# Kernel optimization log

Hardware: AMD Instinct MI355X
Metric: run time of the kernel (lower is better)

The kernel has to match this reference:

```python
import jax, jax.numpy as jnp
import numpy as np

ALPHA = 0.2  # leaky-relu negative slope AND the residual scale self.alpha

def setup_inputs() -> dict:
    key = jax.random.key(0)
    k1, k2, k3 = jax.random.split(key, 3)
    B, N, C_in, C_out = 8, 2048, 128, 128
    text = jax.random.normal(k1, (B, N, C_in), dtype=jnp.float32)
    adj = jnp.ones((B, N, N), dtype=jnp.float32)  # unused by the layer's forward
    W = jax.random.normal(k2, (C_in, C_out), dtype=jnp.float32) * (1.414 / np.sqrt(C_in + C_out))
    a = jax.random.normal(k3, (2 * C_out, 1), dtype=jnp.float32) * (1.414 / np.sqrt(2 * C_out + 1))
    return {"text": text, "adj": adj, "W": W, "a": a}

def reference(text, adj, W, a):
    # text: [B,N,C_in]; adj is unused (faithful to the source forward).
    h = jnp.einsum('bnc,cf->bnf', text, W)                  # [B,N,F]
    F_out = W.shape[1]
    a1 = a[:F_out, 0]                                       # score contribution of node i
    a2 = a[F_out:, 0]                                       # score contribution of node j
    s1 = jnp.einsum('bnf,f->bn', h, a1)                     # [B,N]
    s2 = jnp.einsum('bnf,f->bn', h, a2)                     # [B,N]
    # leakyrelu(cat(h_i,h_j) @ a) == leakyrelu(s1_i + s2_j): avoids O(N^2*2F) concat
    e = jax.nn.leaky_relu(s1[:, :, None] + s2[:, None, :], negative_slope=ALPHA)  # [B,N,N]
    attention = jax.nn.softmax(e, axis=2)                   # dropout is a no-op in eval mode
    h_prime = jnp.einsum('bij,bjf->bif', attention, h)      # [B,N,F]
    return jax.nn.elu(h_prime + ALPHA * h)
```

## Files before the change

kernel.cpp:

```cpp
#include <hip/hip_runtime.h>
#include <hip/hip_bf16.h>
#include <math.h>

#define LRELU_ALPHA 0.2f

constexpr int B_ = 8;
constexpr int N_ = 2048;
constexpr int M_ = B_ * N_;
constexpr int SEG = 32;
constexpr int NSEG = N_ / SEG;

__global__ __launch_bounds__(512) void k_gemm(const float* __restrict__ text,
                                              const float* __restrict__ W,
                                              const float* __restrict__ a,
                                              float* __restrict__ h,
                                              float* __restrict__ s1,
                                              float* __restrict__ s2,
                                              float* __restrict__ eN0,
                                              float* __restrict__ eP0) {
    __shared__ float As[64 * 33];
    __shared__ float Ws[32 * 128];
    const int tid = threadIdx.x;
    const int r0  = blockIdx.x * 64;
    const int cx  = tid & 15;
    const int ry  = tid >> 4;
    const int c0  = cx * 8;
    const int rr0 = ry * 2;

    float acc[2][8];
#pragma unroll
    for (int i = 0; i < 2; ++i)
#pragma unroll
        for (int j = 0; j < 8; ++j) acc[i][j] = 0.f;

    for (int kk = 0; kk < 128; kk += 32) {
        for (int idx = tid; idx < 64 * 32; idx += 512) {
            int r = idx >> 5, c = idx & 31;
            As[r * 33 + c] = text[(r0 + r) * 128 + kk + c];
        }
        for (int idx = tid; idx < 32 * 128; idx += 512) {
            int k = idx >> 7, f = idx & 127;
            Ws[k * 128 + f] = W[(kk + k) * 128 + f];
        }
        __syncthreads();
#pragma unroll
        for (int k = 0; k < 32; ++k) {
            float4 w0 = *(const float4*)&Ws[k * 128 + c0];
            float4 w1 = *(const float4*)&Ws[k * 128 + c0 + 4];
#pragma unroll
            for (int i = 0; i < 2; ++i) {
                float av = As[(rr0 + i) * 33 + k];
                acc[i][0] += av * w0.x; acc[i][1] += av * w0.y;
                acc[i][2] += av * w0.z; acc[i][3] += av * w0.w;
                acc[i][4] += av * w1.x; acc[i][5] += av * w1.y;
                acc[i][6] += av * w1.z; acc[i][7] += av * w1.w;
            }
        }
        __syncthreads();
    }

    float4 a10 = *(const float4*)&a[c0];
    float4 a11 = *(const float4*)&a[c0 + 4];
    float4 a20 = *(const float4*)&a[128 + c0];
    float4 a21 = *(const float4*)&a[128 + c0 + 4];

#pragma unroll
    for (int i = 0; i < 2; ++i) {
        int row = r0 + rr0 + i;
        float4 o0 = {acc[i][0], acc[i][1], acc[i][2], acc[i][3]};
        float4 o1 = {acc[i][4], acc[i][5], acc[i][6], acc[i][7]};
        *(float4*)&h[row * 128 + c0]     = o0;
        *(float4*)&h[row * 128 + c0 + 4] = o1;

        float p1 = o0.x * a10.x + o0.y * a10.y + o0.z * a10.z + o0.w * a10.w
                 + o1.x * a11.x + o1.y * a11.y + o1.z * a11.z + o1.w * a11.w;
        float p2 = o0.x * a20.x + o0.y * a20.y + o0.z * a20.z + o0.w * a20.w
                 + o1.x * a21.x + o1.y * a21.y + o1.z * a21.z + o1.w * a21.w;
#pragma unroll
        for (int off = 8; off >= 1; off >>= 1) {
            p1 += __shfl_xor(p1, off);
            p2 += __shfl_xor(p2, off);
        }
        if (cx == 0) {
            s1[row] = p1;
            s2[row] = p2;
            eN0[row] = expf(LRELU_ALPHA * p2);
            eP0[row] = expf(p2);
        }
    }
}

__global__ __launch_bounds__(512) void k_rank(const float* __restrict__ s2,
                                              const float* __restrict__ eN0,
                                              const float* __restrict__ eP0,
                                              const float* __restrict__ s1,
                                              int* __restrict__ perm,
                                              float* __restrict__ eNs,
                                              float* __restrict__ ePs,
                                              int* __restrict__ rank,
                                              float* __restrict__ ZN,
                                              float* __restrict__ ZP) {
    __shared__ float ls2[2048], leN[2048], leP[2048];
    __shared__ int   redc[512], redm[512];
    __shared__ float redn[512], redp[512];

    const int b  = blockIdx.x >> 5;
    const int eb = blockIdx.x & 31;
    const int tid = threadIdx.x;
    const int e = tid & 63;
    const int c = tid >> 6;

    {
        const float4* g2 = (const float4*)(s2  + b * 2048);
        const float4* gn = (const float4*)(eN0 + b * 2048);
        const float4* gp = (const float4*)(eP0 + b * 2048);
        ((float4*)ls2)[tid] = g2[tid];
        ((float4*)leN)[tid] = gn[tid];
        ((float4*)leP)[tid] = gp[tid];
    }
    __syncthreads();

    const int i  = eb * 64 + e;
    const int gi = b * 2048 + i;
    const float myS2 = ls2[i];
    const float thr  = -s1[gi];

    int cnt = 0, mr = 0;
    float sn = 0.f, sp = 0.f;
    const int j0 = c * 256;
#pragma unroll 4
    for (int j = j0; j < j0 + 256; j += 4) {
        float4 v  = *(const float4*)&ls2[j];
        float4 en = *(const float4*)&leN[j];
        float4 ep = *(const float4*)&leP[j];
#define PROC(vv, ee, pp, jj)                                             \
        { bool le = (vv) <= thr;                                         \
          cnt += le ? 1 : 0;                                             \
          sn  += le ? (ee) : 0.f;                                        \
          sp  += le ? 0.f : (pp);                                        \
          mr  += ((vv) < myS2 || ((vv) == myS2 && (jj) < i)) ? 1 : 0; }
        PROC(v.x, en.x, ep.x, j + 0)
        PROC(v.y, en.y, ep.y, j + 1)
        PROC(v.z, en.z, ep.z, j + 2)
        PROC(v.w, en.w, ep.w, j + 3)
#undef PROC
    }
    redc[tid] = cnt; redm[tid] = mr; redn[tid] = sn; redp[tid] = sp;
    __syncthreads();
    if (c == 0) {
        int tc = 0, tm = 0; float tn = 0.f, tp = 0.f;
#pragma unroll
        for (int cc = 0; cc < 8; ++cc) {
            tc += redc[cc * 64 + e];
            tm += redm[cc * 64 + e];
            tn += redn[cc * 64 + e];
            tp += redp[cc * 64 + e];
        }
        perm[b * 2048 + tm] = i;
        eNs [b * 2048 + tm] = leN[i];
        ePs [b * 2048 + tm] = leP[i];
        rank[gi] = tc;
        ZN[gi] = tn;
        ZP[gi] = tp;
    }
}

__global__ __launch_bounds__(128) void k_segsum(const float* __restrict__ h,
                                                const int* __restrict__ perm,
                                                const float* __restrict__ eNs,
                                                const float* __restrict__ ePs,
                                                float* __restrict__ segN,
                                                float* __restrict__ segP) {
    const int blk = blockIdx.x;
    const int b = blk >> 6, s = blk & 63;
    const int f = threadIdx.x;
    const int rbase = s * SEG;
    float an = 0.f, ap = 0.f;
#pragma unroll 4
    for (int r = 0; r < SEG; ++r) {
        int rr = b * 2048 + rbase + r;
        float hv = h[(b * 2048 + perm[rr]) * 128 + f];
        an += eNs[rr] * hv;
        ap += ePs[rr] * hv;
    }
    segN[blk * 128 + f] = an;
    segP[blk * 128 + f] = ap;
}

__global__ __launch_bounds__(128) void k_prefix(const float* __restrict__ h,
                                                const int* __restrict__ perm,
                                                const float* __restrict__ eNs,
                                                const float* __restrict__ ePs,
                                                const float* __restrict__ segN,
                                                const float* __restrict__ segP,
                                                __hip_bfloat16* __restrict__ Pre,
                                                __hip_bfloat16* __restrict__ Suf) {
    const int blk = blockIdx.x;
    const int b = blk >> 6, s = blk & 63;
    const int f = threadIdx.x;
    const int rbase = s * SEG;

    float an = 0.f, ap = 0.f;
    for (int ss = 0; ss < s; ++ss)        an += segN[(b * NSEG + ss) * 128 + f];
    for (int ss = s + 1; ss < NSEG; ++ss) ap += segP[(b * NSEG + ss) * 128 + f];

    float hv[SEG];
#pragma unroll
    for (int r = 0; r < SEG; ++r) {
        int rr = b * 2048 + rbase + r;
        hv[r] = h[(b * 2048 + perm[rr]) * 128 + f];
        Pre[(size_t)(b * 2049 + rbase + r) * 128 + f] = __float2bfloat16(an);
        an += eNs[rr] * hv[r];
    }
#pragma unroll
    for (int r = SEG - 1; r >= 0; --r) {
        int rr = b * 2048 + rbase + r;
        ap += ePs[rr] * hv[r];
        Suf[(size_t)(b * 2049 + rbase + r) * 128 + f] = __float2bfloat16(ap);
    }
    if (s == NSEG - 1) {
        Pre[(size_t)(b * 2049 + 2048) * 128 + f] = __float2bfloat16(an);
        Suf[(size_t)(b * 2049 + 2048) * 128 + f] = __float2bfloat16(0.f);
    }
}

__global__ __launch_bounds__(256) void k_out(const float* __restrict__ h,
                                             const float* __restrict__ s1,
                                             const int* __restrict__ rank,
                                             const float* __restrict__ ZN,
                                             const float* __restrict__ ZP,
                                             const __hip_bfloat16* __restrict__ Pre,
                                             const __hip_bfloat16* __restrict__ Suf,
                                             float* __restrict__ out) {
    const int tid = threadIdx.x;
    const int lr = tid >> 7, f = tid & 127;
    const int i = blockIdx.x * 2 + lr;
    const int b = i >> 11;

    const float s1v = s1[i];
    const float E1 = expf(s1v);
    const float E2 = expf(LRELU_ALPHA * s1v);
    const int   r  = rank[i];
    const float Z  = E1 * ZP[i] + E2 * ZN[i];
    const size_t o = (size_t)(b * 2049 + r) * 128 + f;
    const float hp = (E1 * __bfloat162float(Suf[o]) + E2 * __bfloat162float(Pre[o])) / Z;
    const float x = hp + LRELU_ALPHA * h[i * 128 + f];
    out[i * 128 + f] = (x > 0.f) ? x : expm1f(x);
}

extern "C" void kernel_launch(void* const* d_in, const int* in_sizes, int n_in,
                              void* d_out, int out_size, void* d_ws, size_t ws_size,
                              hipStream_t stream) {
    const float* text = (const float*)d_in[0];
    const float* W = (const float*)d_in[2];
    const float* a = (const float*)d_in[3];
    float* out = (float*)d_out;

    float* p = (float*)d_ws;
    float* h    = p; p += (size_t)M_ * 128;
    float* s1   = p; p += M_;
    float* s2   = p; p += M_;
    float* eN0  = p; p += M_;
    float* eP0  = p; p += M_;
    int*   perm = (int*)p; p += M_;
    float* eNs  = p; p += M_;
    float* ePs  = p; p += M_;
    int*   rank = (int*)p; p += M_;
    float* ZN   = p; p += M_;
    float* ZP   = p; p += M_;
    float* segN = p; p += B_ * NSEG * 128;
    float* segP = p; p += B_ * NSEG * 128;
    __hip_bfloat16* Pre = (__hip_bfloat16*)p; p += (size_t)B_ * 2049 * 128 / 2;
    __hip_bfloat16* Suf = (__hip_bfloat16*)p; p += (size_t)B_ * 2049 * 128 / 2;

    hipLaunchKernelGGL(k_gemm,   dim3(M_ / 64),   dim3(512), 0, stream,
                       text, W, a, h, s1, s2, eN0, eP0);
    hipLaunchKernelGGL(k_rank,   dim3(B_ * 32),   dim3(512), 0, stream,
                       s2, eN0, eP0, s1, perm, eNs, ePs, rank, ZN, ZP);
    hipLaunchKernelGGL(k_segsum, dim3(B_ * NSEG), dim3(128), 0, stream,
                       h, perm, eNs, ePs, segN, segP);
    hipLaunchKernelGGL(k_prefix, dim3(B_ * NSEG), dim3(128), 0, stream,
                       h, perm, eNs, ePs, segN, segP, Pre, Suf);
    hipLaunchKernelGGL(k_out,    dim3(M_ / 2),    dim3(256), 0, stream,
                       h, s1, rank, ZN, ZP, Pre, Suf, out);
}
```

Measured before the change: 235.4 us.

## Fuse all five stages into one cooperative persistent kernel with grid syncs

Replaces the five separate launches (gemm, rank, segment sums, prefix/suffix scans, output) with a single cooperative kernel of 256 blocks that separates stages with grid-wide syncs and reuses one shared-memory union across phases. The GEMM phase is retiled to 64-wide k chunks with a transposed A tile and 4x8 register tiles, computed by only half the threads. The segment-sum and scan phases are rebalanced so each block handles two segments, with the prefix and suffix scans split across thread halves. The aim is to remove launch gaps and tail effects between kernels, at the cost of grid-sync overhead, idle threads in the GEMM, and only 256 blocks doing the output stage.

```diff
diff --git a/kernel.cpp b/kernel.cpp
--- a/kernel.cpp
+++ b/kernel.cpp
@@ -1,6 +1,9 @@
 #include <hip/hip_runtime.h>
 #include <hip/hip_bf16.h>
+#include <hip/hip_cooperative_groups.h>
 #include <math.h>
+
+namespace cg = cooperative_groups;
 
 #define LRELU_ALPHA 0.2f
 
@@ -10,242 +13,241 @@
 constexpr int SEG = 32;
 constexpr int NSEG = N_ / SEG;
 
-__global__ __launch_bounds__(512) void k_gemm(const float* __restrict__ text,
-                                              const float* __restrict__ W,
-                                              const float* __restrict__ a,
-                                              float* __restrict__ h,
-                                              float* __restrict__ s1,
-                                              float* __restrict__ s2,
-                                              float* __restrict__ eN0,
-                                              float* __restrict__ eP0) {
-    __shared__ float As[64 * 33];
-    __shared__ float Ws[32 * 128];
+__global__ __launch_bounds__(512) void k_fused(
+    const float* __restrict__ text, const float* __restrict__ W,
+    const float* __restrict__ a,
+    float* __restrict__ h, float* __restrict__ s1, float* __restrict__ s2,
+    float* __restrict__ eN0, float* __restrict__ eP0,
+    int* __restrict__ perm, float* __restrict__ eNs, float* __restrict__ ePs,
+    int* __restrict__ rank, float* __restrict__ ZN, float* __restrict__ ZP,
+    float* __restrict__ segN, float* __restrict__ segP,
+    __hip_bfloat16* __restrict__ Pre, __hip_bfloat16* __restrict__ Suf,
+    float* __restrict__ out) {
+
+    __shared__ __align__(16) union {
+        struct { float Ast[64 * 68]; float Ws[64 * 128]; } p1;
+        struct { float ls2[2048], leN[2048], leP[2048];
+                 int redc[512], redm[512]; float redn[512], redp[512]; } p2;
+        struct { float an[512], ap[512]; } p3;
+    } sm;
+
     const int tid = threadIdx.x;
-    const int r0  = blockIdx.x * 64;
-    const int cx  = tid & 15;
-    const int ry  = tid >> 4;
-    const int c0  = cx * 8;
-    const int rr0 = ry * 2;
-
-    float acc[2][8];
-#pragma unroll
-    for (int i = 0; i < 2; ++i)
-#pragma unroll
-        for (int j = 0; j < 8; ++j) acc[i][j] = 0.f;
-
-    for (int kk = 0; kk < 128; kk += 32) {
-        for (int idx = tid; idx < 64 * 32; idx += 512) {
-            int r = idx >> 5, c = idx & 31;
-            As[r * 33 + c] = text[(r0 + r) * 128 + kk + c];
-        }
-        for (int idx = tid; idx < 32 * 128; idx += 512) {
-            int k = idx >> 7, f = idx & 127;
-            Ws[k * 128 + f] = W[(kk + k) * 128 + f];
+    const int blk = blockIdx.x;
+    cg::grid_group grid = cg::this_grid();
+
+    {
+        const int r0 = blk * 64;
+        const int cx = tid & 15;
+        const int ry = tid >> 4;
+        const int c0 = cx * 4;
+        const int c1 = 64 + cx * 4;
+        const int rr0 = ry * 4;
+
+        float acc[4][8];
+#pragma unroll
+        for (int i = 0; i < 4; ++i)
+#pragma unroll
+            for (int j = 0; j < 8; ++j) acc[i][j] = 0.f;
+
+        for (int kk = 0; kk < 128; kk += 64) {
+            for (int idx = tid; idx < 64 * 64; idx += 512) {
+                int r = idx >> 6, k = idx & 63;
+                sm.p1.Ast[k * 68 + r] = text[(size_t)(r0 + r) * 128 + kk + k];
+            }
+            for (int idx = tid; idx < 64 * 128; idx += 512) {
+                int k = idx >> 7, f = idx & 127;
+                sm.p1.Ws[k * 128 + f] = W[(kk + k) * 128 + f];
+            }
+            __syncthreads();
+            if (tid < 256) {
+#pragma unroll 16
+                for (int k = 0; k < 64; ++k) {
+                    float4 av = *(const float4*)&sm.p1.Ast[k * 68 + rr0];
+                    float4 w0 = *(const float4*)&sm.p1.Ws[k * 128 + c0];
+                    float4 w1 = *(const float4*)&sm.p1.Ws[k * 128 + c1];
+                    const float avv[4] = {av.x, av.y, av.z, av.w};
+#pragma unroll
+                    for (int i = 0; i < 4; ++i) {
+                        acc[i][0] += avv[i] * w0.x; acc[i][1] += avv[i] * w0.y;
+                        acc[i][2] += avv[i] * w0.z; acc[i][3] += avv[i] * w0.w;
+                        acc[i][4] += avv[i] * w1.x; acc[i][5] += avv[i] * w1.y;
+                        acc[i][6] += avv[i] * w1.z; acc[i][7] += avv[i] * w1.w;
+                    }
+                }
+            }
+            __syncthreads();
+        }
+
+        if (tid < 256) {
+            float4 a1lo = *(const float4*)&a[c0];
+            float4 a1hi = *(const float4*)&a[c1];
+            float4 a2lo = *(const float4*)&a[128 + c0];
+            float4 a2hi = *(const float4*)&a[128 + c1];
+#pragma unroll
+            for (int i = 0; i < 4; ++i) {
+                const int row = r0 + rr0 + i;
+                float4 o0 = {acc[i][0], acc[i][1], acc[i][2], acc[i][3]};
+                float4 o1 = {acc[i][4], acc[i][5], acc[i][6], acc[i][7]};
+                *(float4*)&h[(size_t)row * 128 + c0] = o0;
+                *(float4*)&h[(size_t)row * 128 + c1] = o1;
+
+                float p1 = o0.x*a1lo.x + o0.y*a1lo.y + o0.z*a1lo.z + o0.w*a1lo.w
+                         + o1.x*a1hi.x + o1.y*a1hi.y + o1.z*a1hi.z + o1.w*a1hi.w;
+                float p2 = o0.x*a2lo.x + o0.y*a2lo.y + o0.z*a2lo.z + o0.w*a2lo.w
+                         + o1.x*a2hi.x + o1.y*a2hi.y + o1.z*a2hi.z + o1.w*a2hi.w;
+#pragma unroll
+                for (int off = 8; off >= 1; off >>= 1) {
+                    p1 += __shfl_xor(p1, off);
+                    p2 += __shfl_xor(p2, off);
+                }
+                if (cx == 0) {
+                    s1[row] = p1;
+                    s2[row] = p2;
+                    eN0[row] = expf(LRELU_ALPHA * p2);
+                    eP0[row] = expf(p2);
+                }
+            }
+        }
+    }
+    grid.sync();
+
+    {
+        const int b  = blk >> 5;
+        const int eb = blk & 31;
+        const int e  = tid & 63;
+        const int c  = tid >> 6;
+        {
+            const float4* g2 = (const float4*)(s2  + b * 2048);
+            const float4* gn = (const float4*)(eN0 + b * 2048);
+            const float4* gp = (const float4*)(eP0 + b * 2048);
+            ((float4*)sm.p2.ls2)[tid] = g2[tid];
+            ((float4*)sm.p2.leN)[tid] = gn[tid];
+            ((float4*)sm.p2.leP)[tid] = gp[tid];
         }
         __syncthreads();
-#pragma unroll
-        for (int k = 0; k < 32; ++k) {
-            float4 w0 = *(const float4*)&Ws[k * 128 + c0];
-            float4 w1 = *(const float4*)&Ws[k * 128 + c0 + 4];
-#pragma unroll
-            for (int i = 0; i < 2; ++i) {
-                float av = As[(rr0 + i) * 33 + k];
-                acc[i][0] += av * w0.x; acc[i][1] += av * w0.y;
-                acc[i][2] += av * w0.z; acc[i][3] += av * w0.w;
-                acc[i][4] += av * w1.x; acc[i][5] += av * w1.y;
-                acc[i][6] += av * w1.z; acc[i][7] += av * w1.w;
-            }
-        }
+
+        const int i  = eb * 64 + e;
+        const int gi = b * 2048 + i;
+        const float myS2 = sm.p2.ls2[i];
+        const float thr  = -s1[gi];
+
+        int cnt = 0, mr = 0;
+        float sn = 0.f, sp = 0.f;
+        const int j0 = c * 256;
+#pragma unroll 4
+        for (int j = j0; j < j0 + 256; j += 4) {
+            float4 v  = *(const float4*)&sm.p2.ls2[j];
+            float4 en = *(const float4*)&sm.p2.leN[j];
+            float4 ep = *(const float4*)&sm.p2.leP[j];
+#define PROC(vv, ee, pp, jj)                                             \
+            { bool le = (vv) <= thr;                                     \
+              cnt += le ? 1 : 0;                                         \
+              sn  += le ? (ee) : 0.f;                                    \
+              sp  += le ? 0.f : (pp);                                    \
+              mr  += ((vv) < myS2 || ((vv) == myS2 && (jj) < i)) ? 1 : 0; }
+            PROC(v.x, en.x, ep.x, j + 0)
+            PROC(v.y, en.y, ep.y, j + 1)
+            PROC(v.z, en.z, ep.z, j + 2)
+            PROC(v.w, en.w, ep.w, j + 3)
+#undef PROC
+        }
+        sm.p2.redc[tid] = cnt; sm.p2.redm[tid] = mr;
+        sm.p2.redn[tid] = sn;  sm.p2.redp[tid] = sp;
         __syncthreads();
-    }
-
-    float4 a10 = *(const float4*)&a[c0];
-    float4 a11 = *(const float4*)&a[c0 + 4];
-    float4 a20 = *(const float4*)&a[128 + c0];
-    float4 a21 = *(const float4*)&a[128 + c0 + 4];
-
-#pragma unroll
-    for (int i = 0; i < 2; ++i) {
-        int row = r0 + rr0 + i;
-        float4 o0 = {acc[i][0], acc[i][1], acc[i][2], acc[i][3]};
-        float4 o1 = {acc[i][4], acc[i][5], acc[i][6], acc[i][7]};
-        *(float4*)&h[row * 128 + c0]     = o0;
-        *(float4*)&h[row * 128 + c0 + 4] = o1;
-
-        float p1 = o0.x * a10.x + o0.y * a10.y + o0.z * a10.z + o0.w * a10.w
-                 + o1.x * a11.x + o1.y * a11.y + o1.z * a11.z + o1.w * a11.w;
-        float p2 = o0.x * a20.x + o0.y * a20.y + o0.z * a20.z + o0.w * a20.w
-                 + o1.x * a21.x + o1.y * a21.y + o1.z * a21.z + o1.w * a21.w;
-#pragma unroll
-        for (int off = 8; off >= 1; off >>= 1) {
-            p1 += __shfl_xor(p1, off);
-            p2 += __shfl_xor(p2, off);
-        }
-        if (cx == 0) {
-            s1[row] = p1;
-            s2[row] = p2;
-            eN0[row] = expf(LRELU_ALPHA * p2);
-            eP0[row] = expf(p2);
-        }
-    }
-}
-
-__global__ __launch_bounds__(512) void k_rank(const float* __restrict__ s2,
-                                              const float* __restrict__ eN0,
-                                              const float* __restrict__ eP0,
-                                              const float* __restrict__ s1,
-                                              int* __restrict__ perm,
-                                              float* __restrict__ eNs,
-                                              float* __restrict__ ePs,
-                                              int* __restrict__ rank,
-                                              float* __restrict__ ZN,
-                                              float* __restrict__ ZP) {
-    __shared__ float ls2[2048], leN[2048], leP[2048];
-    __shared__ int   redc[512], redm[512];
-    __shared__ float redn[512], redp[512];
-
-    const int b  = blockIdx.x >> 5;
-    const int eb = blockIdx.x & 31;
-    const int tid = threadIdx.x;
-    const int e = tid & 63;
-    const int c = tid >> 6;
-
-    {
-        const float4* g2 = (const float4*)(s2  + b * 2048);
-        const float4* gn = (const float4*)(eN0 + b * 2048);
-        const float4* gp = (const float4*)(eP0 + b * 2048);
-        ((float4*)ls2)[tid] = g2[tid];
-        ((float4*)leN)[tid] = gn[tid];
-        ((float4*)leP)[tid] = gp[tid];
-    }
-    __syncthreads();
-
-    const int i  = eb * 64 + e;
-    const int gi = b * 2048 + i;
-    const float myS2 = ls2[i];
-    const float thr  = -s1[gi];
-
-    int cnt = 0, mr = 0;
-    float sn = 0.f, sp = 0.f;
-    const int j0 = c * 256;
-#pragma unroll 4
-    for (int j = j0; j < j0 + 256; j += 4) {
-        float4 v  = *(const float4*)&ls2[j];
-        float4 en = *(const float4*)&leN[j];
-        float4 ep = *(const float4*)&leP[j];
-#define PROC(vv, ee, pp, jj)                                             \
-        { bool le = (vv) <= thr;                                         \
-          cnt += le ? 1 : 0;                                             \
-          sn  += le ? (ee) : 0.f;                                        \
-          sp  += le ? 0.f : (pp);                                        \
-          mr  += ((vv) < myS2 || ((vv) == myS2 && (jj) < i)) ? 1 : 0; }
-        PROC(v.x, en.x, ep.x, j + 0)
-        PROC(v.y, en.y, ep.y, j + 1)
-        PROC(v.z, en.z, ep.z, j + 2)
-        PROC(v.w, en.w, ep.w, j + 3)
-#undef PROC
-    }
-    redc[tid] = cnt; redm[tid] = mr; redn[tid] = sn; redp[tid] = sp;
-    __syncthreads();
-    if (c == 0) {
-        int tc = 0, tm = 0; float tn = 0.f, tp = 0.f;
-#pragma unroll
-        for (int cc = 0; cc < 8; ++cc) {
-            tc += redc[cc * 64 + e];
-            tm += redm[cc * 64 + e];
-            tn += redn[cc * 64 + e];
-            tp += redp[cc * 64 + e];
-        }
-        perm[b * 2048 + tm] = i;
-        eNs [b * 2048 + tm] = leN[i];
-        ePs [b * 2048 + tm] = leP[i];
-        rank[gi] = tc;
-        ZN[gi] = tn;
-        ZP[gi] = tp;
-    }
-}
-
-__global__ __launch_bounds__(128) void k_segsum(const float* __restrict__ h,
-                                                const int* __restrict__ perm,
-                                                const float* __restrict__ eNs,
-                                                const float* __restrict__ ePs,
-                                                float* __restrict__ segN,
-                                                float* __restrict__ segP) {
-    const int blk = blockIdx.x;
-    const int b = blk >> 6, s = blk & 63;
-    const int f = threadIdx.x;
-    const int rbase = s * SEG;
-    float an = 0.f, ap = 0.f;
-#pragma unroll 4
-    for (int r = 0; r < SEG; ++r) {
-        int rr = b * 2048 + rbase + r;
-        float hv = h[(b * 2048 + perm[rr]) * 128 + f];
-        an += eNs[rr] * hv;
-        ap += ePs[rr] * hv;
-    }
-    segN[blk * 128 + f] = an;
-    segP[blk * 128 + f] = ap;
-}
-
-__global__ __launch_bounds__(128) void k_prefix(const float* __restrict__ h,
-                                                const int* __restrict__ perm,
-                                                const float* __restrict__ eNs,
-                                                const float* __restrict__ ePs,
-                                                const float* __restrict__ segN,
-                                                const float* __restrict__ segP,
-                                                __hip_bfloat16* __restrict__ Pre,
-                                                __hip_bfloat16* __restrict__ Suf) {
-    const int blk = blockIdx.x;
-    const int b = blk >> 6, s = blk & 63;
-    const int f = threadIdx.x;
-    const int rbase = s * SEG;
-
-    float an = 0.f, ap = 0.f;
-    for (int ss = 0; ss < s; ++ss)        an += segN[(b * NSEG + ss) * 128 + f];
-    for (int ss = s + 1; ss < NSEG; ++ss) ap += segP[(b * NSEG + ss) * 128 + f];
-
-    float hv[SEG];
-#pragma unroll
-    for (int r = 0; r < SEG; ++r) {
-        int rr = b * 2048 + rbase + r;
-        hv[r] = h[(b * 2048 + perm[rr]) * 128 + f];
-        Pre[(size_t)(b * 2049 + rbase + r) * 128 + f] = __float2bfloat16(an);
-        an += eNs[rr] * hv[r];
-    }
-#pragma unroll
-    for (int r = SEG - 1; r >= 0; --r) {
-        int rr = b * 2048 + rbase + r;
-        ap += ePs[rr] * hv[r];
-        Suf[(size_t)(b * 2049 + rbase + r) * 128 + f] = __float2bfloat16(ap);
-    }
-    if (s == NSEG - 1) {
-        Pre[(size_t)(b * 2049 + 2048) * 128 + f] = __float2bfloat16(an);
-        Suf[(size_t)(b * 2049 + 2048) * 128 + f] = __float2bfloat16(0.f);
-    }
-}
-
-__global__ __launch_bounds__(256) void k_out(const float* __restrict__ h,
-                                             const float* __restrict__ s1,
-                                             const int* __restrict__ rank,
-                                             const float* __restrict__ ZN,
-                                             const float* __restrict__ ZP,
-                                             const __hip_bfloat16* __restrict__ Pre,
-                                             const __hip_bfloat16* __restrict__ Suf,
-                                             float* __restrict__ out) {
-    const int tid = threadIdx.x;
-    const int lr = tid >> 7, f = tid & 127;
-    const int i = blockIdx.x * 2 + lr;
-    const int b = i >> 11;
-
-    const float s1v = s1[i];
-    const float E1 = expf(s1v);
-    const float E2 = expf(LRELU_ALPHA * s1v);
-    const int   r  = rank[i];
-    const float Z  = E1 * ZP[i] + E2 * ZN[i];
-    const size_t o = (size_t)(b * 2049 + r) * 128 + f;
-    const float hp = (E1 * __bfloat162float(Suf[o]) + E2 * __bfloat162float(Pre[o])) / Z;
-    const float x = hp + LRELU_ALPHA * h[i * 128 + f];
-    out[i * 128 + f] = (x > 0.f) ? x : expm1f(x);
+        if (c == 0) {
+            int tc = 0, tm = 0; float tn = 0.f, tp = 0.f;
+#pragma unroll
+            for (int cc = 0; cc < 8; ++cc) {
+                tc += sm.p2.redc[cc * 64 + e];
+                tm += sm.p2.redm[cc * 64 + e];
+                tn += sm.p2.redn[cc * 64 + e];
+                tp += sm.p2.redp[cc * 64 + e];
+            }
+            perm[b * 2048 + tm] = i;
+            eNs [b * 2048 + tm] = sm.p2.leN[i];
+            ePs [b * 2048 + tm] = sm.p2.leP[i];
+            rank[gi] = tc;
+            ZN[gi] = tn;
+            ZP[gi] = tp;
+        }
+    }
+    grid.sync();
+
+    {
+        const int task = blk * 2 + (tid >> 8);
+        const int st = tid & 255;
+        const int f  = st & 127;
+        const int hf = st >> 7;
+        const int b3 = task >> 6, s3 = task & 63;
+        float an = 0.f, ap = 0.f;
+        const int rb = b3 * 2048 + s3 * SEG + hf * 16;
+#pragma unroll 4
+        for (int r = 0; r < 16; ++r) {
+            int rr = rb + r;
+            float hv = h[(size_t)(b3 * 2048 + perm[rr]) * 128 + f];
+            an += eNs[rr] * hv;
+            ap += ePs[rr] * hv;
+        }
+        sm.p3.an[tid] = an; sm.p3.ap[tid] = ap;
+        __syncthreads();
+        if (hf == 0) {
+            segN[task * 128 + f] = sm.p3.an[tid] + sm.p3.an[tid + 128];
+            segP[task * 128 + f] = sm.p3.ap[tid] + sm.p3.ap[tid + 128];
+        }
+    }
+    grid.sync();
+
+    {
+        const int task = blk * 2 + (tid >> 8);
+        const int st = tid & 255;
+        const int f  = st & 127;
+        const int hf = st >> 7;
+        const int b4 = task >> 6, s4 = task & 63;
+        const int rbase = s4 * SEG;
+        if (hf == 0) {
+            float an = 0.f;
+            for (int ss = 0; ss < s4; ++ss) an += segN[(b4 * NSEG + ss) * 128 + f];
+#pragma unroll 4
+            for (int r = 0; r < SEG; ++r) {
+                int rr = b4 * 2048 + rbase + r;
+                Pre[(size_t)(b4 * 2049 + rbase + r) * 128 + f] = __float2bfloat16(an);
+                an += eNs[rr] * h[(size_t)(b4 * 2048 + perm[rr]) * 128 + f];
+            }
+            if (s4 == NSEG - 1)
+                Pre[(size_t)(b4 * 2049 + 2048) * 128 + f] = __float2bfloat16(an);
+        } else {
+            float ap = 0.f;
+            for (int ss = s4 + 1; ss < NSEG; ++ss) ap += segP[(b4 * NSEG + ss) * 128 + f];
+#pragma unroll 4
+            for (int r = SEG - 1; r >= 0; --r) {
+                int rr = b4 * 2048 + rbase + r;
+                ap += ePs[rr] * h[(size_t)(b4 * 2048 + perm[rr]) * 128 + f];
+                Suf[(size_t)(b4 * 2049 + rbase + r) * 128 + f] = __float2bfloat16(ap);
+            }
+            if (s4 == NSEG - 1)
+                Suf[(size_t)(b4 * 2049 + 2048) * 128 + f] = __float2bfloat16(0.f);
+        }
+    }
+    grid.sync();
+
+    {
+        const int lr = tid >> 7;
+        const int f  = tid & 127;
+#pragma unroll 2
+        for (int it = 0; it < 16; ++it) {
+            const int i = blk * 64 + it * 4 + lr;
+            const int b = i >> 11;
+            const float s1v = s1[i];
+            const float E1 = expf(s1v);
+            const float E2 = expf(LRELU_ALPHA * s1v);
+            const int   r  = rank[i];
+            const float Z  = E1 * ZP[i] + E2 * ZN[i];
+            const size_t o = (size_t)(b * 2049 + r) * 128 + f;
+            const float hp = (E1 * __bfloat162float(Suf[o]) + E2 * __bfloat162float(Pre[o])) / Z;
+            const float x = hp + LRELU_ALPHA * h[(size_t)i * 128 + f];
+            out[(size_t)i * 128 + f] = (x > 0.f) ? x : expm1f(x);
+        }
+    }
 }
 
 extern "C" void kernel_launch(void* const* d_in, const int* in_sizes, int n_in,
@@ -273,14 +275,9 @@
     __hip_bfloat16* Pre = (__hip_bfloat16*)p; p += (size_t)B_ * 2049 * 128 / 2;
     __hip_bfloat16* Suf = (__hip_bfloat16*)p; p += (size_t)B_ * 2049 * 128 / 2;
 
-    hipLaunchKernelGGL(k_gemm,   dim3(M_ / 64),   dim3(512), 0, stream,
-                       text, W, a, h, s1, s2, eN0, eP0);
-    hipLaunchKernelGGL(k_rank,   dim3(B_ * 32),   dim3(512), 0, stream,
-                       s2, eN0, eP0, s1, perm, eNs, ePs, rank, ZN, ZP);
-    hipLaunchKernelGGL(k_segsum, dim3(B_ * NSEG), dim3(128), 0, stream,
-                       h, perm, eNs, ePs, segN, segP);
-    hipLaunchKernelGGL(k_prefix, dim3(B_ * NSEG), dim3(128), 0, stream,
-                       h, perm, eNs, ePs, segN, segP, Pre, Suf);
-    hipLaunchKernelGGL(k_out,    dim3(M_ / 2),    dim3(256), 0, stream,
-                       h, s1, rank, ZN, ZP, Pre, Suf, out);
+    void* args[] = { &text, &W, &a, &h, &s1, &s2, &eN0, &eP0,
+                     &perm, &eNs, &ePs, &rank, &ZN, &ZP,
+                     &segN, &segP, &Pre, &Suf, &out };
+    hipLaunchCooperativeKernel((void*)k_fused, dim3(256), dim3(512),
+                               args, 0, stream);
 }
```

Result: slower. 350.4 us (+48.9%).
